# Kernel optimization log

Measured on AMD Instinct MI355X. Metric: run time of the kernel, lower is better.

Reference implementation:

```python
import jax, jax.numpy as jnp
import numpy as np

EMBED_DIM = 64
N_EMBED = 1024
BATCH, H, W = 16, 64, 64


def setup_inputs() -> dict:
    key = jax.random.key(0)
    k1, k2 = jax.random.split(key)
    inputs = jax.random.normal(k1, (BATCH, H, W, EMBED_DIM), dtype=jnp.float32)
    # codebook as in Quantize.build: RandomNormal(stddev=1.0), shape (embed_dim, n_embed)
    cluster_mean = jax.random.normal(k2, (EMBED_DIM, N_EMBED), dtype=jnp.float32)
    return {"inputs": inputs, "cluster_mean": cluster_mean}


def reference(inputs, cluster_mean):
    # inputs: [B,H,W,D]; cluster_mean: [D,K]
    D = cluster_mean.shape[0]
    samples = inputs.reshape(-1, D)  # [N,D]
    dist = (
        jnp.sum(samples * samples, axis=1, keepdims=True)
        - 2.0 * (samples @ cluster_mean)
        + jnp.sum(cluster_mean * cluster_mean, axis=0, keepdims=True)
    )
    cluster_index = jnp.argmin(dist, axis=1).reshape(inputs.shape[:-1])  # [B,H,W]
    quantize = cluster_mean.T[cluster_index]  # gather -> [B,H,W,D]
    q_loss = jnp.mean((quantize - jax.lax.stop_gradient(inputs)) ** 2)
    e_loss = jnp.mean((jax.lax.stop_gradient(quantize) - inputs) ** 2)
    loss = q_loss + 0.25 * e_loss
    # straight-through estimator
    outputs = inputs + jax.lax.stop_gradient(quantize - inputs)
    return outputs, cluster_index, loss
```

## Files before the change

kernel.cpp:

```cpp
#include <hip/hip_runtime.h>
#include <stdint.h>

#define NS 65536
#define D 64
#define K 1024
#define NEL 4194304
#define MARGIN_KEY 0.025f

typedef short bf16x8 __attribute__((ext_vector_type(8)));
typedef float f32x4 __attribute__((ext_vector_type(4)));
typedef float f32x16 __attribute__((ext_vector_type(16)));

static __device__ __forceinline__ unsigned short bf16_rne(float x) {
    union { float f; uint32_t u; } v; v.f = x;
    uint32_t r = v.u + 0x7FFFu + ((v.u >> 16) & 1u);
    return (unsigned short)(r >> 16);
}
static __device__ __forceinline__ float bf16f(unsigned short h) {
    union { uint32_t u; float f; } v; v.u = ((uint32_t)h) << 16;
    return v.f;
}

__global__ __launch_bounds__(256) void vq_prep(
    const float* __restrict__ cm,
    unsigned short* __restrict__ P,
    float* __restrict__ cnorm,
    double* __restrict__ acc,
    unsigned int* __restrict__ cnt)
{
    const int tx = threadIdx.x;
    const int c  = tx & 31;
    const int dg = tx >> 5;
    const int t  = blockIdx.x;
    const int k  = t * 32 + c;
    if (t == 0 && tx == 0) { *acc = 0.0; *cnt = 0u; }

    float p = 0.f;
    bf16x8 hv, lv;
#pragma unroll
    for (int j = 0; j < 8; ++j) {
        float v = cm[(dg * 8 + j) * K + k];
        unsigned short hb = bf16_rne(v);
        hv[j] = (short)hb;
        lv[j] = (short)bf16_rne(v - bf16f(hb));
        p = fmaf(v, v, p);
    }
    const int s = dg >> 1, kh = dg & 1;
    *(bf16x8*)(P + ((size_t)(t * 8 + s) * 64 + kh * 32 + c) * 8)     = hv;
    *(bf16x8*)(P + ((size_t)(t * 8 + 4 + s) * 64 + kh * 32 + c) * 8) = lv;

    __shared__ float pn[32][9];
    pn[c][dg] = p;
    __syncthreads();
    if (tx < 32) {
        float sm = 0.f;
#pragma unroll
        for (int g = 0; g < 8; ++g) sm += pn[tx][g];
        cnorm[t * 32 + tx] = sm;
    }
}

__global__ __launch_bounds__(256, 2) void vq_main(
    const float* __restrict__ xin,
    const float* __restrict__ cm,
    const unsigned short* __restrict__ P,
    const float* __restrict__ cnorm,
    float* __restrict__ outq,
    float* __restrict__ outidx,
    double* __restrict__ acc_g,
    unsigned int* __restrict__ cnt_g,
    float* __restrict__ loss_out)
{
    __shared__ char smemA[36864];
    __shared__ unsigned short ring[4][4096];
    __shared__ float cn_lds[1024];
    __shared__ int   widx[128];

    unsigned short* xh = (unsigned short*)smemA;
    unsigned short* xl = (unsigned short*)(smemA + 18432);
    float* mb1 = (float*)smemA;
    float* mb2 = (float*)(smemA + 16896);
    float* red = (float*)smemA;

    const int tx = threadIdx.x;
    const int S0 = blockIdx.x * 128;
    const int w = tx >> 6, l = tx & 63;

#define ISSUE(T) do {                                                          \
        const unsigned short* g_ = P + (size_t)(T) * 4096 + tx * 8;            \
        __builtin_amdgcn_global_load_lds(g_, &ring[(T) & 3][tx * 8], 16, 0, 0);\
        __builtin_amdgcn_global_load_lds(g_ + 2048, &ring[(T) & 3][2048 + tx * 8], 16, 0, 0); \
    } while (0)
#define WAITV(N) asm volatile("s_waitcnt vmcnt(" #N ")" ::: "memory")

    ISSUE(0); ISSUE(1); ISSUE(2);

    {
        const int sr = tx >> 1, dh = (tx & 1) * 32;
        const float* gp = xin + (size_t)(S0 + sr) * D + dh;
#pragma unroll
        for (int g = 0; g < 2; ++g) {
            bf16x8 hv0, hv1, lv0, lv1;
#pragma unroll
            for (int j = 0; j < 8; ++j) {
                float va = gp[g * 16 + j], vb = gp[g * 16 + 8 + j];
                unsigned short ha = bf16_rne(va), hb = bf16_rne(vb);
                hv0[j] = (short)ha; hv1[j] = (short)hb;
                lv0[j] = (short)bf16_rne(va - bf16f(ha));
                lv1[j] = (short)bf16_rne(vb - bf16f(hb));
            }
            *(bf16x8*)(xh + sr * 72 + dh + g * 16)     = hv0;
            *(bf16x8*)(xh + sr * 72 + dh + g * 16 + 8) = hv1;
            *(bf16x8*)(xl + sr * 72 + dh + g * 16)     = lv0;
            *(bf16x8*)(xl + sr * 72 + dh + g * 16 + 8) = lv1;
        }
#pragma unroll
        for (int q = 0; q < 4; ++q)
            cn_lds[q * 256 + tx] = 0.5f * cnorm[q * 256 + tx];
    }
    __syncthreads();

    const int arow = w * 32 + (l & 31);
    const int kh8 = (l >> 5) * 8;
    bf16x8 AH0 = *(const bf16x8*)(xh + arow * 72 + 0  + kh8);
    bf16x8 AH1 = *(const bf16x8*)(xh + arow * 72 + 16 + kh8);
    bf16x8 AH2 = *(const bf16x8*)(xh + arow * 72 + 32 + kh8);
    bf16x8 AH3 = *(const bf16x8*)(xh + arow * 72 + 48 + kh8);
    bf16x8 AL0 = *(const bf16x8*)(xl + arow * 72 + 0  + kh8);
    bf16x8 AL1 = *(const bf16x8*)(xl + arow * 72 + 16 + kh8);
    bf16x8 AL2 = *(const bf16x8*)(xl + arow * 72 + 32 + kh8);
    bf16x8 AL3 = *(const bf16x8*)(xl + arow * 72 + 48 + kh8);

    float b1[16], b2[16];
#pragma unroll
    for (int j = 0; j < 16; ++j) { b1[j] = 3.4e38f; b2[j] = 3.4e38f; }

    const f32x16 Z16 = {0.f,0.f,0.f,0.f,0.f,0.f,0.f,0.f,
                        0.f,0.f,0.f,0.f,0.f,0.f,0.f,0.f};

#define BODY(T) do {                                                           \
        const unsigned short* bt_ = &ring[(T) & 3][0];                         \
        bf16x8 Bh0 = *(const bf16x8*)(bt_ + 0    + l * 8);                     \
        bf16x8 Bh1 = *(const bf16x8*)(bt_ + 512  + l * 8);                     \
        bf16x8 Bh2 = *(const bf16x8*)(bt_ + 1024 + l * 8);                     \
        bf16x8 Bh3 = *(const bf16x8*)(bt_ + 1536 + l * 8);                     \
        bf16x8 Bl0 = *(const bf16x8*)(bt_ + 2048 + l * 8);                     \
        bf16x8 Bl1 = *(const bf16x8*)(bt_ + 2560 + l * 8);                     \
        bf16x8 Bl2 = *(const bf16x8*)(bt_ + 3072 + l * 8);                     \
        bf16x8 Bl3 = *(const bf16x8*)(bt_ + 3584 + l * 8);                     \
        f32x16 a_ = Z16;                                                       \
        a_ = __builtin_amdgcn_mfma_f32_32x32x16_bf16(AH0, Bh0, a_, 0, 0, 0);   \
        a_ = __builtin_amdgcn_mfma_f32_32x32x16_bf16(AH1, Bh1, a_, 0, 0, 0);   \
        a_ = __builtin_amdgcn_mfma_f32_32x32x16_bf16(AH2, Bh2, a_, 0, 0, 0);   \
        a_ = __builtin_amdgcn_mfma_f32_32x32x16_bf16(AH3, Bh3, a_, 0, 0, 0);   \
        a_ = __builtin_amdgcn_mfma_f32_32x32x16_bf16(AH0, Bl0, a_, 0, 0, 0);   \
        a_ = __builtin_amdgcn_mfma_f32_32x32x16_bf16(AH1, Bl1, a_, 0, 0, 0);   \
        a_ = __builtin_amdgcn_mfma_f32_32x32x16_bf16(AH2, Bl2, a_, 0, 0, 0);   \
        a_ = __builtin_amdgcn_mfma_f32_32x32x16_bf16(AH3, Bl3, a_, 0, 0, 0);   \
        a_ = __builtin_amdgcn_mfma_f32_32x32x16_bf16(AL0, Bh0, a_, 0, 0, 0);   \
        a_ = __builtin_amdgcn_mfma_f32_32x32x16_bf16(AL1, Bh1, a_, 0, 0, 0);   \
        a_ = __builtin_amdgcn_mfma_f32_32x32x16_bf16(AL2, Bh2, a_, 0, 0, 0);   \
        a_ = __builtin_amdgcn_mfma_f32_32x32x16_bf16(AL3, Bh3, a_, 0, 0, 0);   \
        const float ch_ = cn_lds[(T) * 32 + (l & 31)];                         \
        const unsigned tt_ = (unsigned)(T);                                    \
        _Pragma("unroll")                                                      \
        for (int j = 0; j < 16; ++j) {                                         \
            float k_ = ch_ - a_[j];                                            \
            unsigned pu_ = (__builtin_bit_cast(unsigned, k_) & 0xFFFFFFC0u) | tt_; \
            float f_ = __builtin_bit_cast(float, pu_);                         \
            b2[j] = __builtin_amdgcn_fmed3f(b1[j], f_, b2[j]);                 \
            b1[j] = fminf(b1[j], f_);                                          \
        }                                                                      \
    } while (0)

    for (int t = 0; t < 29; ++t) {
        WAITV(4);
        __builtin_amdgcn_s_barrier();
        ISSUE(t + 3);
        BODY(t);
    }
    WAITV(4); __builtin_amdgcn_s_barrier(); BODY(29);
    WAITV(2); __builtin_amdgcn_s_barrier(); BODY(30);
    WAITV(0); __builtin_amdgcn_s_barrier(); BODY(31);

    {
        const int cc = l & 31, hh = l >> 5;
#pragma unroll
        for (int j = 0; j < 16; ++j) {
            const int r = (j & 3) + 8 * (j >> 2) + 4 * hh;
            const int sr2 = w * 32 + r;
            mb1[sr2 * 33 + cc] = b1[j];
            mb2[sr2 * 33 + cc] = b2[j];
        }
    }
    __syncthreads();

    if (tx < 128) {
        float B1 = 3.4e38f, B2 = 3.4e38f; int I1 = 0, I2 = 0;
#pragma unroll
        for (int c = 0; c < 32; ++c) {
            float v1 = mb1[tx * 33 + c];
            float v2 = mb2[tx * 33 + c];
            int j1 = (int)(__builtin_bit_cast(unsigned, v1) & 63u) * 32 + c;
            int j2 = (int)(__builtin_bit_cast(unsigned, v2) & 63u) * 32 + c;
            if (v1 < B1)      { B2 = B1; I2 = I1; B1 = v1; I1 = j1; }
            else if (v1 < B2) { B2 = v1; I2 = j1; }
            if (v2 < B1)      { B2 = B1; I2 = I1; B1 = v2; I1 = j2; }
            else if (v2 < B2) { B2 = v2; I2 = j2; }
        }
        int winner = I1;
        if (B2 - B1 < MARGIN_KEY) {
            const float* xp = xin + (size_t)(S0 + tx) * D;
            float a0 = 0, a1 = 0, a2 = 0, a3 = 0, e0 = 0, e1 = 0, e2 = 0, e3 = 0;
            for (int dd = 0; dd < D; dd += 4) {
                float x0 = xp[dd], x1 = xp[dd + 1], x2 = xp[dd + 2], x3 = xp[dd + 3];
                a0 = fmaf(x0, cm[(dd + 0) * K + I1], a0);
                a1 = fmaf(x1, cm[(dd + 1) * K + I1], a1);
                a2 = fmaf(x2, cm[(dd + 2) * K + I1], a2);
                a3 = fmaf(x3, cm[(dd + 3) * K + I1], a3);
                e0 = fmaf(x0, cm[(dd + 0) * K + I2], e0);
                e1 = fmaf(x1, cm[(dd + 1) * K + I2], e1);
                e2 = fmaf(x2, cm[(dd + 2) * K + I2], e2);
                e3 = fmaf(x3, cm[(dd + 3) * K + I2], e3);
            }
            float d1 = cn_lds[I1] - ((a0 + a1) + (a2 + a3));
            float d2 = cn_lds[I2] - ((e0 + e1) + (e2 + e3));
            if (d2 < d1 || (d2 == d1 && I2 < I1)) winner = I2;
        }
        widx[tx] = winner;
    }
    __syncthreads();

    float psum = 0.f;
#pragma unroll
    for (int half = 0; half < 2; ++half) {
        const int sl = (tx >> 2) + half * 64, d0 = (tx & 3) * 16;
        const int gs = S0 + sl;
        const int wi = widx[sl];
        const int gt = wi >> 5, gc = wi & 31;
        const int s4 = d0 >> 4;
        const unsigned short* gh = P + ((size_t)(gt * 8 + s4) * 64 + gc) * 8;
        const unsigned short* gl = P + ((size_t)(gt * 8 + 4 + s4) * 64 + gc) * 8;
        bf16x8 h0 = *(const bf16x8*)(gh);
        bf16x8 h1 = *(const bf16x8*)(gh + 256);
        bf16x8 l0 = *(const bf16x8*)(gl);
        bf16x8 l1 = *(const bf16x8*)(gl + 256);
        const float* xr = xin + (size_t)gs * D + d0;
        float* oq = outq + (size_t)gs * D + d0;
#pragma unroll
        for (int g = 0; g < 4; ++g) {
            float4 xv = *(const float4*)(xr + 4 * g);
            float q0 = bf16f((unsigned short)(g < 2 ? h0[4 * g + 0] : h1[4 * g - 8 + 0])) +
                       bf16f((unsigned short)(g < 2 ? l0[4 * g + 0] : l1[4 * g - 8 + 0]));
            float q1 = bf16f((unsigned short)(g < 2 ? h0[4 * g + 1] : h1[4 * g - 8 + 1])) +
                       bf16f((unsigned short)(g < 2 ? l0[4 * g + 1] : l1[4 * g - 8 + 1]));
            float q2 = bf16f((unsigned short)(g < 2 ? h0[4 * g + 2] : h1[4 * g - 8 + 2])) +
                       bf16f((unsigned short)(g < 2 ? l0[4 * g + 2] : l1[4 * g - 8 + 2]));
            float q3 = bf16f((unsigned short)(g < 2 ? h0[4 * g + 3] : h1[4 * g - 8 + 3])) +
                       bf16f((unsigned short)(g < 2 ? l0[4 * g + 3] : l1[4 * g - 8 + 3]));
            float dx = q0 - xv.x, dy = q1 - xv.y, dz = q2 - xv.z, dw = q3 - xv.w;
            float4 o;
            o.x = xv.x + dx; o.y = xv.y + dy; o.z = xv.z + dz; o.w = xv.w + dw;
            *(float4*)(oq + 4 * g) = o;
            psum = fmaf(dx, dx, psum);
            psum = fmaf(dy, dy, psum);
            psum = fmaf(dz, dz, psum);
            psum = fmaf(dw, dw, psum);
        }
    }

    if (tx < 128)
        outidx[S0 + tx] = (float)widx[tx];

    __syncthreads();
    red[tx] = psum;
    __syncthreads();
    for (int st = 128; st > 0; st >>= 1) {
        if (tx < st) red[tx] += red[tx + st];
        __syncthreads();
    }
    if (tx == 0) {
        atomicAdd(acc_g, (double)red[0]);
        __threadfence();
        unsigned prev = atomicAdd(cnt_g, 1u);
        if (prev == gridDim.x - 1) {
            __threadfence();
            double a = atomicAdd(acc_g, 0.0);
            float m = (float)(a / (double)NEL);
            *loss_out = m + 0.25f * m;
        }
    }
#undef ISSUE
#undef WAITV
#undef BODY
}

extern "C" void kernel_launch(void* const* d_in, const int* in_sizes, int n_in,
                              void* d_out, int out_size, void* d_ws, size_t ws_size,
                              hipStream_t stream) {
    const float* xin = (const float*)d_in[0];
    const float* cm  = (const float*)d_in[1];

    float* out     = (float*)d_out;
    float* outq    = out;
    float* outidx  = out + NEL;
    float* outloss = out + NEL + NS;

    unsigned short* P = (unsigned short*)d_ws;
    float*  cnorm = (float*)((char*)d_ws + 262144);
    double* acc   = (double*)((char*)d_ws + 266240);
    unsigned int* cnt = (unsigned int*)((char*)d_ws + 266248);

    vq_prep<<<32, 256, 0, stream>>>(cm, P, cnorm, acc, cnt);
    vq_main<<<512, 256, 0, stream>>>(xin, cm, P, cnorm, outq, outidx,
                                     acc, cnt, outloss);
}
```

Measured before the change: 132.5 us.

## Keep codebook resident in registers and stream sample tiles through LDS

The main kernel is restructured so each wave holds a fixed slice of the split bf16 codebook in registers and streams 32-sample tiles of inputs through a double-buffered LDS buffer. The codebook norm term is folded into the MFMA accumulation via an extra bf16 hi/lo operand built in the prep kernel. Argmax top-2 tracking now uses explicit indices, with a cross-wave merge in LDS. Blocks grow to 512 threads covering 256 samples. This removes the per-block streaming of the whole codebook through an LDS ring, at the cost of heavy register pressure, a larger LDS footprint and a barrier per sample tile.

```diff
diff --git a/kernel.cpp b/kernel.cpp
--- a/kernel.cpp
+++ b/kernel.cpp
@@ -24,6 +24,7 @@
 __global__ __launch_bounds__(256) void vq_prep(
     const float* __restrict__ cm,
     unsigned short* __restrict__ P,
+    unsigned short* __restrict__ P2,
     float* __restrict__ cnorm,
     double* __restrict__ acc,
     unsigned int* __restrict__ cnt)
@@ -57,13 +58,26 @@
 #pragma unroll
         for (int g = 0; g < 8; ++g) sm += pn[tx][g];
         cnorm[t * 32 + tx] = sm;
-    }
-}
-
-__global__ __launch_bounds__(256, 2) void vq_main(
+        unsigned short chi = bf16_rne(-0.5f * sm);
+        unsigned short clo = bf16_rne(-0.5f * sm - bf16f(chi));
+        bf16x8 a;
+#pragma unroll
+        for (int j = 0; j < 8; ++j) a[j] = 0;
+        a[0] = (short)chi; a[1] = (short)clo;
+        *(bf16x8*)(P2 + (size_t)t * 512 + tx * 8) = a;
+    } else if (tx < 64) {
+        bf16x8 a;
+#pragma unroll
+        for (int j = 0; j < 8; ++j) a[j] = 0;
+        *(bf16x8*)(P2 + (size_t)t * 512 + tx * 8) = a;
+    }
+}
+
+__global__ __launch_bounds__(512, 2) void vq_main(
     const float* __restrict__ xin,
     const float* __restrict__ cm,
     const unsigned short* __restrict__ P,
+    const unsigned short* __restrict__ P2,
     const float* __restrict__ cnorm,
     float* __restrict__ outq,
     float* __restrict__ outidx,
@@ -71,145 +85,151 @@
     unsigned int* __restrict__ cnt_g,
     float* __restrict__ loss_out)
 {
-    __shared__ char smemA[36864];
-    __shared__ unsigned short ring[4][4096];
-    __shared__ float cn_lds[1024];
-    __shared__ int   widx[128];
-
-    unsigned short* xh = (unsigned short*)smemA;
-    unsigned short* xl = (unsigned short*)(smemA + 18432);
-    float* mb1 = (float*)smemA;
-    float* mb2 = (float*)(smemA + 16896);
-    float* red = (float*)smemA;
+    __shared__ unsigned short xb[8192];
+    __shared__ float pt1[256 * 17];
+    __shared__ float pt2[256 * 17];
+    __shared__ int   pi1[256 * 17];
+    __shared__ int   pi2[256 * 17];
+    __shared__ int   widx[256];
+    __shared__ float red[512];
 
     const int tx = threadIdx.x;
-    const int S0 = blockIdx.x * 128;
+    const int S0 = blockIdx.x * 256;
     const int w = tx >> 6, l = tx & 63;
 
-#define ISSUE(T) do {                                                          \
-        const unsigned short* g_ = P + (size_t)(T) * 4096 + tx * 8;            \
-        __builtin_amdgcn_global_load_lds(g_, &ring[(T) & 3][tx * 8], 16, 0, 0);\
-        __builtin_amdgcn_global_load_lds(g_ + 2048, &ring[(T) & 3][2048 + tx * 8], 16, 0, 0); \
-    } while (0)
-#define WAITV(N) asm volatile("s_waitcnt vmcnt(" #N ")" ::: "memory")
-
-    ISSUE(0); ISSUE(1); ISSUE(2);
-
-    {
-        const int sr = tx >> 1, dh = (tx & 1) * 32;
-        const float* gp = xin + (size_t)(S0 + sr) * D + dh;
-#pragma unroll
-        for (int g = 0; g < 2; ++g) {
-            bf16x8 hv0, hv1, lv0, lv1;
-#pragma unroll
-            for (int j = 0; j < 8; ++j) {
-                float va = gp[g * 16 + j], vb = gp[g * 16 + 8 + j];
-                unsigned short ha = bf16_rne(va), hb = bf16_rne(vb);
-                hv0[j] = (short)ha; hv1[j] = (short)hb;
-                lv0[j] = (short)bf16_rne(va - bf16f(ha));
-                lv1[j] = (short)bf16_rne(vb - bf16f(hb));
-            }
-            *(bf16x8*)(xh + sr * 72 + dh + g * 16)     = hv0;
-            *(bf16x8*)(xh + sr * 72 + dh + g * 16 + 8) = hv1;
-            *(bf16x8*)(xl + sr * 72 + dh + g * 16)     = lv0;
-            *(bf16x8*)(xl + sr * 72 + dh + g * 16 + 8) = lv1;
-        }
-#pragma unroll
-        for (int q = 0; q < 4; ++q)
-            cn_lds[q * 256 + tx] = 0.5f * cnorm[q * 256 + tx];
-    }
-    __syncthreads();
-
-    const int arow = w * 32 + (l & 31);
-    const int kh8 = (l >> 5) * 8;
-    bf16x8 AH0 = *(const bf16x8*)(xh + arow * 72 + 0  + kh8);
-    bf16x8 AH1 = *(const bf16x8*)(xh + arow * 72 + 16 + kh8);
-    bf16x8 AH2 = *(const bf16x8*)(xh + arow * 72 + 32 + kh8);
-    bf16x8 AH3 = *(const bf16x8*)(xh + arow * 72 + 48 + kh8);
-    bf16x8 AL0 = *(const bf16x8*)(xl + arow * 72 + 0  + kh8);
-    bf16x8 AL1 = *(const bf16x8*)(xl + arow * 72 + 16 + kh8);
-    bf16x8 AL2 = *(const bf16x8*)(xl + arow * 72 + 32 + kh8);
-    bf16x8 AL3 = *(const bf16x8*)(xl + arow * 72 + 48 + kh8);
-
-    float b1[16], b2[16];
-#pragma unroll
-    for (int j = 0; j < 16; ++j) { b1[j] = 3.4e38f; b2[j] = 3.4e38f; }
+    bf16x8 CH[4][4], CL[4][4], A4[4];
+#pragma unroll
+    for (int t = 0; t < 4; ++t) {
+#pragma unroll
+        for (int s = 0; s < 4; ++s) {
+            CH[t][s] = *(const bf16x8*)(P + ((size_t)((w * 4 + t) * 8 + s) * 64 + l) * 8);
+            CL[t][s] = *(const bf16x8*)(P + ((size_t)((w * 4 + t) * 8 + 4 + s) * 64 + l) * 8);
+        }
+        A4[t] = *(const bf16x8*)(P2 + (size_t)(w * 4 + t) * 512 + l * 8);
+    }
+    bf16x8 B4;
+#pragma unroll
+    for (int j = 0; j < 8; ++j) B4[j] = 0;
+    if (l < 32) { B4[0] = (short)0x3F80; B4[1] = (short)0x3F80; }
+
+    if (tx < 256) {
+        const int ss = tx >> 6, sll = tx & 63;
+        const int skh = sll >> 5, ssp = sll & 31;
+        const float* gp = xin + (size_t)(S0 + ssp) * D + ss * 16 + skh * 8;
+        bf16x8 h8, l8;
+#pragma unroll
+        for (int j = 0; j < 8; ++j) {
+            float v = gp[j];
+            unsigned short hb = bf16_rne(v);
+            h8[j] = (short)hb;
+            l8[j] = (short)bf16_rne(v - bf16f(hb));
+        }
+        *(bf16x8*)(xb + (0 * 4 + ss) * 512 + sll * 8) = h8;
+        *(bf16x8*)(xb + (1 * 4 + ss) * 512 + sll * 8) = l8;
+    }
 
     const f32x16 Z16 = {0.f,0.f,0.f,0.f,0.f,0.f,0.f,0.f,
                         0.f,0.f,0.f,0.f,0.f,0.f,0.f,0.f};
-
-#define BODY(T) do {                                                           \
-        const unsigned short* bt_ = &ring[(T) & 3][0];                         \
-        bf16x8 Bh0 = *(const bf16x8*)(bt_ + 0    + l * 8);                     \
-        bf16x8 Bh1 = *(const bf16x8*)(bt_ + 512  + l * 8);                     \
-        bf16x8 Bh2 = *(const bf16x8*)(bt_ + 1024 + l * 8);                     \
-        bf16x8 Bh3 = *(const bf16x8*)(bt_ + 1536 + l * 8);                     \
-        bf16x8 Bl0 = *(const bf16x8*)(bt_ + 2048 + l * 8);                     \
-        bf16x8 Bl1 = *(const bf16x8*)(bt_ + 2560 + l * 8);                     \
-        bf16x8 Bl2 = *(const bf16x8*)(bt_ + 3072 + l * 8);                     \
-        bf16x8 Bl3 = *(const bf16x8*)(bt_ + 3584 + l * 8);                     \
-        f32x16 a_ = Z16;                                                       \
-        a_ = __builtin_amdgcn_mfma_f32_32x32x16_bf16(AH0, Bh0, a_, 0, 0, 0);   \
-        a_ = __builtin_amdgcn_mfma_f32_32x32x16_bf16(AH1, Bh1, a_, 0, 0, 0);   \
-        a_ = __builtin_amdgcn_mfma_f32_32x32x16_bf16(AH2, Bh2, a_, 0, 0, 0);   \
-        a_ = __builtin_amdgcn_mfma_f32_32x32x16_bf16(AH3, Bh3, a_, 0, 0, 0);   \
-        a_ = __builtin_amdgcn_mfma_f32_32x32x16_bf16(AH0, Bl0, a_, 0, 0, 0);   \
-        a_ = __builtin_amdgcn_mfma_f32_32x32x16_bf16(AH1, Bl1, a_, 0, 0, 0);   \
-        a_ = __builtin_amdgcn_mfma_f32_32x32x16_bf16(AH2, Bl2, a_, 0, 0, 0);   \
-        a_ = __builtin_amdgcn_mfma_f32_32x32x16_bf16(AH3, Bl3, a_, 0, 0, 0);   \
-        a_ = __builtin_amdgcn_mfma_f32_32x32x16_bf16(AL0, Bh0, a_, 0, 0, 0);   \
-        a_ = __builtin_amdgcn_mfma_f32_32x32x16_bf16(AL1, Bh1, a_, 0, 0, 0);   \
-        a_ = __builtin_amdgcn_mfma_f32_32x32x16_bf16(AL2, Bh2, a_, 0, 0, 0);   \
-        a_ = __builtin_amdgcn_mfma_f32_32x32x16_bf16(AL3, Bh3, a_, 0, 0, 0);   \
-        const float ch_ = cn_lds[(T) * 32 + (l & 31)];                         \
-        const unsigned tt_ = (unsigned)(T);                                    \
+    const int ibase = w * 128 + 4 * (l >> 5);
+
+    __syncthreads();
+
+#define MFMA32(A, B, C) __builtin_amdgcn_mfma_f32_32x32x16_bf16(A, B, C, 0, 0, 0)
+#define PAIR(T0, T1) do {                                                      \
+        f32x16 a0_ = MFMA32(A4[T0], B4, Z16);                                  \
+        f32x16 a1_ = MFMA32(A4[T1], B4, Z16);                                  \
         _Pragma("unroll")                                                      \
-        for (int j = 0; j < 16; ++j) {                                         \
-            float k_ = ch_ - a_[j];                                            \
-            unsigned pu_ = (__builtin_bit_cast(unsigned, k_) & 0xFFFFFFC0u) | tt_; \
-            float f_ = __builtin_bit_cast(float, pu_);                         \
-            b2[j] = __builtin_amdgcn_fmed3f(b1[j], f_, b2[j]);                 \
-            b1[j] = fminf(b1[j], f_);                                          \
+        for (int s = 0; s < 4; ++s) {                                          \
+            a0_ = MFMA32(CH[T0][s], Bh[s], a0_);                               \
+            a1_ = MFMA32(CH[T1][s], Bh[s], a1_);                               \
+        }                                                                      \
+        _Pragma("unroll")                                                      \
+        for (int s = 0; s < 4; ++s) {                                          \
+            a0_ = MFMA32(CL[T0][s], Bh[s], a0_);                               \
+            a1_ = MFMA32(CL[T1][s], Bh[s], a1_);                               \
+        }                                                                      \
+        _Pragma("unroll")                                                      \
+        for (int s = 0; s < 4; ++s) {                                          \
+            a0_ = MFMA32(CH[T0][s], Bl[s], a0_);                               \
+            a1_ = MFMA32(CH[T1][s], Bl[s], a1_);                               \
+        }                                                                      \
+        _Pragma("unroll")                                                      \
+        for (int r = 0; r < 16; ++r) {                                         \
+            const int ro_ = (r & 3) + 8 * (r >> 2);                            \
+            float v0_ = a0_[r];                                                \
+            const int ix0_ = ibase + (T0) * 32 + ro_;                          \
+            bool c1_ = v0_ > b1, c2_ = v0_ > b2;                               \
+            b2 = __builtin_amdgcn_fmed3f(b1, v0_, b2);                         \
+            b1 = fmaxf(b1, v0_);                                               \
+            i2 = c1_ ? i1 : (c2_ ? ix0_ : i2);                                 \
+            i1 = c1_ ? ix0_ : i1;                                              \
+            float v1_ = a1_[r];                                                \
+            const int ix1_ = ibase + (T1) * 32 + ro_;                          \
+            bool d1_ = v1_ > b1, d2_ = v1_ > b2;                               \
+            b2 = __builtin_amdgcn_fmed3f(b1, v1_, b2);                         \
+            b1 = fmaxf(b1, v1_);                                               \
+            i2 = d1_ ? i1 : (d2_ ? ix1_ : i2);                                 \
+            i1 = d1_ ? ix1_ : i1;                                              \
         }                                                                      \
     } while (0)
 
-    for (int t = 0; t < 29; ++t) {
-        WAITV(4);
-        __builtin_amdgcn_s_barrier();
-        ISSUE(t + 3);
-        BODY(t);
-    }
-    WAITV(4); __builtin_amdgcn_s_barrier(); BODY(29);
-    WAITV(2); __builtin_amdgcn_s_barrier(); BODY(30);
-    WAITV(0); __builtin_amdgcn_s_barrier(); BODY(31);
-
-    {
-        const int cc = l & 31, hh = l >> 5;
-#pragma unroll
-        for (int j = 0; j < 16; ++j) {
-            const int r = (j & 3) + 8 * (j >> 2) + 4 * hh;
-            const int sr2 = w * 32 + r;
-            mb1[sr2 * 33 + cc] = b1[j];
-            mb2[sr2 * 33 + cc] = b2[j];
-        }
-    }
-    __syncthreads();
-
-    if (tx < 128) {
-        float B1 = 3.4e38f, B2 = 3.4e38f; int I1 = 0, I2 = 0;
-#pragma unroll
-        for (int c = 0; c < 32; ++c) {
-            float v1 = mb1[tx * 33 + c];
-            float v2 = mb2[tx * 33 + c];
-            int j1 = (int)(__builtin_bit_cast(unsigned, v1) & 63u) * 32 + c;
-            int j2 = (int)(__builtin_bit_cast(unsigned, v2) & 63u) * 32 + c;
-            if (v1 < B1)      { B2 = B1; I2 = I1; B1 = v1; I1 = j1; }
-            else if (v1 < B2) { B2 = v1; I2 = j1; }
-            if (v2 < B1)      { B2 = B1; I2 = I1; B1 = v2; I1 = j2; }
-            else if (v2 < B2) { B2 = v2; I2 = j2; }
+    for (int st = 0; st < 8; ++st) {
+        const int b = st & 1;
+        bf16x8 Bh[4], Bl[4];
+#pragma unroll
+        for (int s = 0; s < 4; ++s) {
+            Bh[s] = *(const bf16x8*)(xb + ((b * 2 + 0) * 4 + s) * 512 + l * 8);
+            Bl[s] = *(const bf16x8*)(xb + ((b * 2 + 1) * 4 + s) * 512 + l * 8);
+        }
+        float4 xv0, xv1;
+        const int ss = tx >> 6, sll = tx & 63;
+        const int skh = sll >> 5, ssp = sll & 31;
+        if (tx < 256 && st < 7) {
+            const float* gp = xin + (size_t)(S0 + (st + 1) * 32 + ssp) * D
+                              + ss * 16 + skh * 8;
+            xv0 = *(const float4*)(gp);
+            xv1 = *(const float4*)(gp + 4);
+        }
+
+        float b1 = -3.4e38f, b2 = -3.4e38f;
+        int i1 = 0, i2 = 0;
+        PAIR(0, 1);
+        PAIR(2, 3);
+
+        const int si = st * 32 + (l & 31);
+        const int sp = w * 2 + (l >> 5);
+        pt1[si * 17 + sp] = b1;  pi1[si * 17 + sp] = i1;
+        pt2[si * 17 + sp] = b2;  pi2[si * 17 + sp] = i2;
+
+        if (tx < 256 && st < 7) {
+            bf16x8 h8, l8;
+            float vv[8] = {xv0.x, xv0.y, xv0.z, xv0.w, xv1.x, xv1.y, xv1.z, xv1.w};
+#pragma unroll
+            for (int j = 0; j < 8; ++j) {
+                unsigned short hb = bf16_rne(vv[j]);
+                h8[j] = (short)hb;
+                l8[j] = (short)bf16_rne(vv[j] - bf16f(hb));
+            }
+            const int nb = b ^ 1;
+            *(bf16x8*)(xb + ((nb * 2 + 0) * 4 + ss) * 512 + sll * 8) = h8;
+            *(bf16x8*)(xb + ((nb * 2 + 1) * 4 + ss) * 512 + sll * 8) = l8;
+        }
+        __syncthreads();
+    }
+
+    if (tx < 256) {
+        float B1 = -3.4e38f, B2 = -3.4e38f; int I1 = 0, I2 = 0;
+#pragma unroll
+        for (int p = 0; p < 16; ++p) {
+            float v1 = pt1[tx * 17 + p];  int j1 = pi1[tx * 17 + p];
+            float v2 = pt2[tx * 17 + p];  int j2 = pi2[tx * 17 + p];
+            if (v1 > B1)      { B2 = B1; I2 = I1; B1 = v1; I1 = j1; }
+            else if (v1 > B2) { B2 = v1; I2 = j1; }
+            if (v2 > B1)      { B2 = B1; I2 = I1; B1 = v2; I1 = j2; }
+            else if (v2 > B2) { B2 = v2; I2 = j2; }
         }
         int winner = I1;
-        if (B2 - B1 < MARGIN_KEY) {
+        if (B1 - B2 < MARGIN_KEY) {
             const float* xp = xin + (size_t)(S0 + tx) * D;
             float a0 = 0, a1 = 0, a2 = 0, a3 = 0, e0 = 0, e1 = 0, e2 = 0, e3 = 0;
             for (int dd = 0; dd < D; dd += 4) {
@@ -223,60 +243,62 @@
                 e2 = fmaf(x2, cm[(dd + 2) * K + I2], e2);
                 e3 = fmaf(x3, cm[(dd + 3) * K + I2], e3);
             }
-            float d1 = cn_lds[I1] - ((a0 + a1) + (a2 + a3));
-            float d2 = cn_lds[I2] - ((e0 + e1) + (e2 + e3));
-            if (d2 < d1 || (d2 == d1 && I2 < I1)) winner = I2;
+            float k1 = ((a0 + a1) + (a2 + a3)) - 0.5f * cnorm[I1];
+            float k2 = ((e0 + e1) + (e2 + e3)) - 0.5f * cnorm[I2];
+            if (k2 > k1 || (k2 == k1 && I2 < I1)) winner = I2;
         }
         widx[tx] = winner;
     }
     __syncthreads();
 
     float psum = 0.f;
-#pragma unroll
-    for (int half = 0; half < 2; ++half) {
-        const int sl = (tx >> 2) + half * 64, d0 = (tx & 3) * 16;
+    {
+        const int sl = tx >> 1;
+        const int wi = widx[sl];
+        const int gt = wi >> 5, row = wi & 31;
         const int gs = S0 + sl;
-        const int wi = widx[sl];
-        const int gt = wi >> 5, gc = wi & 31;
-        const int s4 = d0 >> 4;
-        const unsigned short* gh = P + ((size_t)(gt * 8 + s4) * 64 + gc) * 8;
-        const unsigned short* gl = P + ((size_t)(gt * 8 + 4 + s4) * 64 + gc) * 8;
-        bf16x8 h0 = *(const bf16x8*)(gh);
-        bf16x8 h1 = *(const bf16x8*)(gh + 256);
-        bf16x8 l0 = *(const bf16x8*)(gl);
-        bf16x8 l1 = *(const bf16x8*)(gl + 256);
-        const float* xr = xin + (size_t)gs * D + d0;
-        float* oq = outq + (size_t)gs * D + d0;
-#pragma unroll
-        for (int g = 0; g < 4; ++g) {
-            float4 xv = *(const float4*)(xr + 4 * g);
-            float q0 = bf16f((unsigned short)(g < 2 ? h0[4 * g + 0] : h1[4 * g - 8 + 0])) +
-                       bf16f((unsigned short)(g < 2 ? l0[4 * g + 0] : l1[4 * g - 8 + 0]));
-            float q1 = bf16f((unsigned short)(g < 2 ? h0[4 * g + 1] : h1[4 * g - 8 + 1])) +
-                       bf16f((unsigned short)(g < 2 ? l0[4 * g + 1] : l1[4 * g - 8 + 1]));
-            float q2 = bf16f((unsigned short)(g < 2 ? h0[4 * g + 2] : h1[4 * g - 8 + 2])) +
-                       bf16f((unsigned short)(g < 2 ? l0[4 * g + 2] : l1[4 * g - 8 + 2]));
-            float q3 = bf16f((unsigned short)(g < 2 ? h0[4 * g + 3] : h1[4 * g - 8 + 3])) +
-                       bf16f((unsigned short)(g < 2 ? l0[4 * g + 3] : l1[4 * g - 8 + 3]));
-            float dx = q0 - xv.x, dy = q1 - xv.y, dz = q2 - xv.z, dw = q3 - xv.w;
-            float4 o;
-            o.x = xv.x + dx; o.y = xv.y + dy; o.z = xv.z + dz; o.w = xv.w + dw;
-            *(float4*)(oq + 4 * g) = o;
-            psum = fmaf(dx, dx, psum);
-            psum = fmaf(dy, dy, psum);
-            psum = fmaf(dz, dz, psum);
-            psum = fmaf(dw, dw, psum);
-        }
-    }
-
-    if (tx < 128)
+#pragma unroll
+        for (int g2 = 0; g2 < 2; ++g2) {
+            const int d0 = (tx & 1) * 32 + g2 * 16;
+            const int s4 = d0 >> 4;
+            const unsigned short* gh = P + ((size_t)(gt * 8 + s4) * 64 + row) * 8;
+            const unsigned short* gl = P + ((size_t)(gt * 8 + 4 + s4) * 64 + row) * 8;
+            bf16x8 h0 = *(const bf16x8*)(gh);
+            bf16x8 h1 = *(const bf16x8*)(gh + 256);
+            bf16x8 l0 = *(const bf16x8*)(gl);
+            bf16x8 l1 = *(const bf16x8*)(gl + 256);
+            const float* xr = xin + (size_t)gs * D + d0;
+            float* oq = outq + (size_t)gs * D + d0;
+#pragma unroll
+            for (int g = 0; g < 4; ++g) {
+                float4 xv = *(const float4*)(xr + 4 * g);
+                float q0 = bf16f((unsigned short)(g < 2 ? h0[4*g+0] : h1[4*g-8+0])) +
+                           bf16f((unsigned short)(g < 2 ? l0[4*g+0] : l1[4*g-8+0]));
+                float q1 = bf16f((unsigned short)(g < 2 ? h0[4*g+1] : h1[4*g-8+1])) +
+                           bf16f((unsigned short)(g < 2 ? l0[4*g+1] : l1[4*g-8+1]));
+                float q2 = bf16f((unsigned short)(g < 2 ? h0[4*g+2] : h1[4*g-8+2])) +
+                           bf16f((unsigned short)(g < 2 ? l0[4*g+2] : l1[4*g-8+2]));
+                float q3 = bf16f((unsigned short)(g < 2 ? h0[4*g+3] : h1[4*g-8+3])) +
+                           bf16f((unsigned short)(g < 2 ? l0[4*g+3] : l1[4*g-8+3]));
+                float dx = q0 - xv.x, dy = q1 - xv.y, dz = q2 - xv.z, dw = q3 - xv.w;
+                float4 o;
+                o.x = xv.x + dx; o.y = xv.y + dy; o.z = xv.z + dz; o.w = xv.w + dw;
+                *(float4*)(oq + 4 * g) = o;
+                psum = fmaf(dx, dx, psum);
+                psum = fmaf(dy, dy, psum);
+                psum = fmaf(dz, dz, psum);
+                psum = fmaf(dw, dw, psum);
+            }
+        }
+    }
+
+    if (tx < 256)
         outidx[S0 + tx] = (float)widx[tx];
 
-    __syncthreads();
     red[tx] = psum;
     __syncthreads();
-    for (int st = 128; st > 0; st >>= 1) {
-        if (tx < st) red[tx] += red[tx + st];
+    for (int st2 = 256; st2 > 0; st2 >>= 1) {
+        if (tx < st2) red[tx] += red[tx + st2];
         __syncthreads();
     }
     if (tx == 0) {
@@ -290,9 +312,8 @@
             *loss_out = m + 0.25f * m;
         }
     }
-#undef ISSUE
-#undef WAITV
-#undef BODY
+#undef PAIR
+#undef MFMA32
 }
 
 extern "C" void kernel_launch(void* const* d_in, const int* in_sizes, int n_in,
@@ -306,12 +327,13 @@
     float* outidx  = out + NEL;
     float* outloss = out + NEL + NS;
 
-    unsigned short* P = (unsigned short*)d_ws;
+    unsigned short* P  = (unsigned short*)d_ws;
     float*  cnorm = (float*)((char*)d_ws + 262144);
-    double* acc   = (double*)((char*)d_ws + 266240);
-    unsigned int* cnt = (unsigned int*)((char*)d_ws + 266248);
-
-    vq_prep<<<32, 256, 0, stream>>>(cm, P, cnorm, acc, cnt);
-    vq_main<<<512, 256, 0, stream>>>(xin, cm, P, cnorm, outq, outidx,
+    unsigned short* P2 = (unsigned short*)((char*)d_ws + 266240);
+    double* acc   = (double*)((char*)d_ws + 299008);
+    unsigned int* cnt = (unsigned int*)((char*)d_ws + 299016);
+
+    vq_prep<<<32, 256, 0, stream>>>(cm, P, P2, cnorm, acc, cnt);
+    vq_main<<<256, 512, 0, stream>>>(xin, cm, P, P2, cnorm, outq, outidx,
                                      acc, cnt, outloss);
 }
```

New measurement: 168.2 us. 27.0% more time.
